# Kernel tuning notes

Hardware: AMD Instinct MI355X
Metric: run time of the kernel (lower is better)

## Reference

```python
import jax, jax.numpy as jnp
import numpy as np

NUM_V = 500_000      # num (k-1)-simplices (vertices)
NUM_E = 1_500_000    # num k-simplices (edges)
NNZ = 2 * NUM_E      # 2 oriented incidences per edge
D_FEAT = 64


def setup_inputs() -> dict:
    key = jax.random.key(0)
    k1, k2, k3, k4 = jax.random.split(key, 4)
    simplex_features = jax.random.normal(k1, (NUM_E, D_FEAT), dtype=jnp.float32)
    # oriented incidence values are +/-1
    boundary_values = jnp.sign(jax.random.normal(k2, (NNZ,), dtype=jnp.float32))
    boundary_values = jnp.where(boundary_values == 0, 1.0, boundary_values)
    boundary_rows = jax.random.randint(k3, (NNZ,), 0, NUM_V, dtype=jnp.int32)
    boundary_cols = jax.random.randint(k4, (NNZ,), 0, NUM_E, dtype=jnp.int32)
    return {
        "simplex_features": simplex_features,
        "boundary_values": boundary_values,
        "boundary_rows": boundary_rows,
        "boundary_cols": boundary_cols,
        "num_out": NUM_V,
    }


def reference(simplex_features, boundary_values, boundary_rows, boundary_cols, num_out):
    # SpMM: out[r, :] += val * features[c, :] over all nonzeros (r, c, val).
    gathered = boundary_values[:, None] * simplex_features[boundary_cols]  # [nnz, d]
    out = jax.ops.segment_sum(gathered, boundary_rows, num_segments=num_out)  # [num_out, d]
    return out
```

## Files before the change

### kernel.cpp

```cpp
#include <hip/hip_runtime.h>

#define D_FEAT 64
#define SCAN_BLOCK 256
#define SCAN_ITEMS 16
#define SCAN_CHUNK (SCAN_BLOCK * SCAN_ITEMS)
#define SCANB_THREADS 1024

#define EMPTY_SLOT 0xFFFFFFFFu
#define ROW_CAP 16

typedef unsigned int u32;
typedef float f4 __attribute__((ext_vector_type(4)));


__device__ __forceinline__ void slow_claim(u32* __restrict__ line, u32 entry, u32 h,
                                           u32 r, u32* __restrict__ spill,
                                           u32* __restrict__ spill_cnt, u32 spill_cap) {
    for (u32 p = 1; p < ROW_CAP; ++p) {
        u32 old = atomicCAS(line + ((h + p) & (ROW_CAP - 1)), EMPTY_SLOT, entry);
        if (old == EMPTY_SLOT) return;
    }
    u32 kk = atomicAdd(spill_cnt, 1u);
    if (kk < spill_cap) { spill[2 * kk] = r; spill[2 * kk + 1] = entry; }
}

__global__ __launch_bounds__(256) void scatter_cas_kernel(
    const int* __restrict__ rows, const int* __restrict__ cols,
    const float* __restrict__ vals, u32* __restrict__ slots,
    u32* __restrict__ spill, u32* __restrict__ spill_cnt, int nnz, u32 spill_cap) {
    long long i4 = (long long)blockIdx.x * blockDim.x + threadIdx.x;
    long long base = i4 * 4;
    if (base >= nnz) return;

    if (base + 3 < nnz) {
        int4 rr = *(const int4*)(rows + base);
        int4 cc = *(const int4*)(cols + base);
        float4 vv = *(const float4*)(vals + base);

        u32 e0 = (u32)cc.x | (vv.x < 0.f ? 0x80000000u : 0u);
        u32 e1 = (u32)cc.y | (vv.y < 0.f ? 0x80000000u : 0u);
        u32 e2 = (u32)cc.z | (vv.z < 0.f ? 0x80000000u : 0u);
        u32 e3 = (u32)cc.w | (vv.w < 0.f ? 0x80000000u : 0u);

        u32* L0 = slots + (size_t)rr.x * ROW_CAP;
        u32* L1 = slots + (size_t)rr.y * ROW_CAP;
        u32* L2 = slots + (size_t)rr.z * ROW_CAP;
        u32* L3 = slots + (size_t)rr.w * ROW_CAP;

        u32 h0 = (u32)(base + 0) & (ROW_CAP - 1);
        u32 h1 = (u32)(base + 1) & (ROW_CAP - 1);
        u32 h2 = (u32)(base + 2) & (ROW_CAP - 1);
        u32 h3 = (u32)(base + 3) & (ROW_CAP - 1);

        u32 o0 = atomicCAS(L0 + h0, EMPTY_SLOT, e0);
        u32 o1 = atomicCAS(L1 + h1, EMPTY_SLOT, e1);
        u32 o2 = atomicCAS(L2 + h2, EMPTY_SLOT, e2);
        u32 o3 = atomicCAS(L3 + h3, EMPTY_SLOT, e3);

        if (o0 != EMPTY_SLOT) slow_claim(L0, e0, h0, (u32)rr.x, spill, spill_cnt, spill_cap);
        if (o1 != EMPTY_SLOT) slow_claim(L1, e1, h1, (u32)rr.y, spill, spill_cnt, spill_cap);
        if (o2 != EMPTY_SLOT) slow_claim(L2, e2, h2, (u32)rr.z, spill, spill_cnt, spill_cap);
        if (o3 != EMPTY_SLOT) slow_claim(L3, e3, h3, (u32)rr.w, spill, spill_cnt, spill_cap);
    } else {
        for (int k = 0; k < 4; ++k) {
            long long e = base + k;
            if (e >= nnz) break;
            int r = rows[e];
            u32 entry = (u32)cols[e] | (vals[e] < 0.f ? 0x80000000u : 0u);
            u32* line = slots + (size_t)r * ROW_CAP;
            u32 h = (u32)e & (ROW_CAP - 1);
            u32 old = atomicCAS(line + h, EMPTY_SLOT, entry);
            if (old != EMPTY_SLOT) slow_claim(line, entry, h, (u32)r, spill, spill_cnt, spill_cap);
        }
    }
}

__global__ __launch_bounds__(256) void gather_cas_kernel(
    const f4* __restrict__ feat4, const u32* __restrict__ slots,
    f4* __restrict__ out4, int numV) {
    long long tid = (long long)blockIdx.x * blockDim.x + threadIdx.x;
    long long wid = tid >> 6;
    int lane = (int)(tid & 63);
    int g = lane >> 4;
    int s = lane & 15;
    long long row = wid * 4 + g;
    if (row >= numV) return;

    const u32* line = slots + row * (long long)ROW_CAP;
    uint4 q0 = *(const uint4*)(line + 0);
    uint4 q1 = *(const uint4*)(line + 4);
    uint4 q2 = *(const uint4*)(line + 8);
    uint4 q3 = *(const uint4*)(line + 12);

    const f4 z = {0.f, 0.f, 0.f, 0.f};
    f4 acc = z;

#define GATHER8(Ea, Eb, Ec, Ed, Ee, Ef, Eg2, Eh)                                   \
    {                                                                              \
        f4 fa = z, fb = z, fc = z, fd = z, fe = z, ff = z, fg = z, fh = z;         \
        if (Ea != EMPTY_SLOT) fa = feat4[(size_t)(Ea & 0x7fffffffu) * 16 + s];     \
        if (Eb != EMPTY_SLOT) fb = feat4[(size_t)(Eb & 0x7fffffffu) * 16 + s];     \
        if (Ec != EMPTY_SLOT) fc = feat4[(size_t)(Ec & 0x7fffffffu) * 16 + s];     \
        if (Ed != EMPTY_SLOT) fd = feat4[(size_t)(Ed & 0x7fffffffu) * 16 + s];     \
        if (Ee != EMPTY_SLOT) fe = feat4[(size_t)(Ee & 0x7fffffffu) * 16 + s];     \
        if (Ef != EMPTY_SLOT) ff = feat4[(size_t)(Ef & 0x7fffffffu) * 16 + s];     \
        if (Eg2 != EMPTY_SLOT) fg = feat4[(size_t)(Eg2 & 0x7fffffffu) * 16 + s];   \
        if (Eh != EMPTY_SLOT) fh = feat4[(size_t)(Eh & 0x7fffffffu) * 16 + s];     \
        acc += fa * ((Ea >> 31) ? -1.f : 1.f);                                     \
        acc += fb * ((Eb >> 31) ? -1.f : 1.f);                                     \
        acc += fc * ((Ec >> 31) ? -1.f : 1.f);                                     \
        acc += fd * ((Ed >> 31) ? -1.f : 1.f);                                     \
        acc += fe * ((Ee >> 31) ? -1.f : 1.f);                                     \
        acc += ff * ((Ef >> 31) ? -1.f : 1.f);                                     \
        acc += fg * ((Eg2 >> 31) ? -1.f : 1.f);                                    \
        acc += fh * ((Eh >> 31) ? -1.f : 1.f);                                     \
    }
    GATHER8(q0.x, q0.y, q0.z, q0.w, q1.x, q1.y, q1.z, q1.w)
    GATHER8(q2.x, q2.y, q2.z, q2.w, q3.x, q3.y, q3.z, q3.w)
#undef GATHER8

    __builtin_nontemporal_store(acc, &out4[row * 16 + s]);
}

__global__ __launch_bounds__(256) void spill_apply_kernel(
    const float* __restrict__ feat, const u32* __restrict__ spill,
    const u32* __restrict__ spill_cnt, float* __restrict__ out, u32 spill_cap) {
    u32 total = *spill_cnt;
    if (total > spill_cap) total = spill_cap;
    int lane = threadIdx.x & 63;
    u32 wid = (blockIdx.x * blockDim.x + threadIdx.x) >> 6;
    u32 nw = (gridDim.x * blockDim.x) >> 6;
    for (u32 i = wid; i < total; i += nw) {
        u32 r = spill[2 * i];
        u32 e = spill[2 * i + 1];
        float f = feat[(size_t)(e & 0x7fffffffu) * D_FEAT + lane];
        atomicAdd(&out[(size_t)r * D_FEAT + lane], (e & 0x80000000u) ? -f : f);
    }
}


__global__ __launch_bounds__(256) void count_kernel(const int* __restrict__ rows,
                                                    u32* __restrict__ cnt, int nnz) {
    int e = blockIdx.x * blockDim.x + threadIdx.x;
    if (e < nnz) atomicAdd(&cnt[rows[e]], 1u);
}

__global__ __launch_bounds__(SCAN_BLOCK) void scanA_kernel(const u32* __restrict__ cnt,
                                                           u32* __restrict__ bsums, int n) {
    int t = threadIdx.x, b = blockIdx.x;
    int i0 = b * SCAN_CHUNK + t * SCAN_ITEMS;
    u32 s = 0;
#pragma unroll
    for (int k = 0; k < SCAN_ITEMS; ++k) {
        int i = i0 + k;
        if (i < n) s += cnt[i];
    }
    __shared__ u32 red[SCAN_BLOCK];
    red[t] = s;
    __syncthreads();
    for (int d = SCAN_BLOCK / 2; d > 0; d >>= 1) {
        if (t < d) red[t] += red[t + d];
        __syncthreads();
    }
    if (t == 0) bsums[b] = red[0];
}

__global__ __launch_bounds__(SCANB_THREADS) void scanB_kernel(u32* __restrict__ bsums, int nb,
                                                              u32* __restrict__ off, int numV,
                                                              u32 nnz) {
    int t = threadIdx.x;
    __shared__ u32 tmp[SCANB_THREADS];
    u32 v = (t < nb) ? bsums[t] : 0u;
    tmp[t] = v;
    __syncthreads();
    for (int d = 1; d < SCANB_THREADS; d <<= 1) {
        u32 x = (t >= d) ? tmp[t - d] : 0u;
        __syncthreads();
        tmp[t] += x;
        __syncthreads();
    }
    if (t < nb) bsums[t] = tmp[t] - v;
    if (t == 0) off[numV] = nnz;
}

__global__ __launch_bounds__(SCAN_BLOCK) void scanC_kernel(const u32* __restrict__ cnt,
                                                           const u32* __restrict__ bsums,
                                                           u32* __restrict__ off,
                                                           u32* __restrict__ cursor, int n) {
    int t = threadIdx.x, b = blockIdx.x;
    int i0 = b * SCAN_CHUNK + t * SCAN_ITEMS;
    u32 s = 0;
#pragma unroll
    for (int k = 0; k < SCAN_ITEMS; ++k) {
        int i = i0 + k;
        if (i < n) s += cnt[i];
    }
    __shared__ u32 tmp[SCAN_BLOCK];
    tmp[t] = s;
    __syncthreads();
    for (int d = 1; d < SCAN_BLOCK; d <<= 1) {
        u32 x = (t >= d) ? tmp[t - d] : 0u;
        __syncthreads();
        tmp[t] += x;
        __syncthreads();
    }
    u32 run = bsums[b] + (tmp[t] - s);
    for (int k = 0; k < SCAN_ITEMS; ++k) {
        int i = i0 + k;
        if (i < n) {
            off[i] = run;
            cursor[i] = run;
            run += cnt[i];
        }
    }
}

__global__ __launch_bounds__(256) void scatter_kernel(const int* __restrict__ rows,
                                                      const int* __restrict__ cols,
                                                      const float* __restrict__ vals,
                                                      u32* __restrict__ cursor,
                                                      u32* __restrict__ packed, int nnz) {
    int e = blockIdx.x * blockDim.x + threadIdx.x;
    if (e >= nnz) return;
    int r = rows[e];
    u32 pos = atomicAdd(&cursor[r], 1u);
    u32 entry = (u32)cols[e] | (vals[e] < 0.f ? 0x80000000u : 0u);
    packed[pos] = entry;
}

__global__ __launch_bounds__(256) void gather_kernel(const float* __restrict__ feat,
                                                     const u32* __restrict__ off,
                                                     const u32* __restrict__ packed,
                                                     float* __restrict__ out, int numV) {
    long long tid = (long long)blockIdx.x * blockDim.x + threadIdx.x;
    long long wid = tid >> 6;
    int lane = (int)(tid & 63);
    if (wid >= numV) return;

    u32 s = off[wid];
    u32 e = off[wid + 1];
    float acc = 0.f;

    for (u32 base = s; base < e; base += 64) {
        int cnt = (int)min(64u, e - base);
        u32 ent = (lane < cnt) ? packed[base + lane] : 0u;
        for (int j0 = 0; j0 < cnt; j0 += 4) {
            float f[4], sg[4];
#pragma unroll
            for (int k = 0; k < 4; ++k) {
                int j = j0 + k;
                u32 ej = __shfl(ent, j);
                long long c = (long long)(ej & 0x7fffffffu);
                sg[k] = (ej >> 31) ? -1.f : 1.f;
                f[k] = (j < cnt) ? feat[c * D_FEAT + lane] : 0.f;
            }
#pragma unroll
            for (int k = 0; k < 4; ++k) acc = fmaf(sg[k], f[k], acc);
        }
    }
    out[wid * D_FEAT + lane] = acc;
}

__global__ __launch_bounds__(256) void atomic_fallback_kernel(
    const float* __restrict__ feat, const float* __restrict__ vals,
    const int* __restrict__ rows, const int* __restrict__ cols,
    float* __restrict__ out, long long nnz) {
    long long tid = (long long)blockIdx.x * blockDim.x + threadIdx.x;
    long long e = tid >> 6;
    int d = (int)(tid & 63);
    if (e >= nnz) return;
    float f = feat[(long long)cols[e] * D_FEAT + d];
    atomicAdd(out + (long long)rows[e] * D_FEAT + d, vals[e] * f);
}

extern "C" void kernel_launch(void* const* d_in, const int* in_sizes, int n_in,
                              void* d_out, int out_size, void* d_ws, size_t ws_size,
                              hipStream_t stream) {
    const float* feat = (const float*)d_in[0];
    const float* vals = (const float*)d_in[1];
    const int*   rows = (const int*)d_in[2];
    const int*   cols = (const int*)d_in[3];
    float*       out  = (float*)d_out;

    int nnz  = in_sizes[1];
    int numV = out_size / D_FEAT;

    {
        const u32 spcap = 1u << 20;
        size_t needT1 = (16 + (size_t)numV * ROW_CAP + 2 * (size_t)spcap) * sizeof(u32);
        if (ws_size >= needT1) {
            u32* ws        = (u32*)d_ws;
            u32* spill_cnt = ws;
            u32* slots     = ws + 16;
            u32* spill     = slots + (size_t)numV * ROW_CAP;

            hipMemsetAsync(spill_cnt, 0, 16 * sizeof(u32), stream);
            hipMemsetAsync(slots, 0xFF, (size_t)numV * ROW_CAP * sizeof(u32), stream);

            long long nth4 = ((long long)nnz + 3) / 4;
            int nb4 = (int)((nth4 + 255) / 256);
            scatter_cas_kernel<<<nb4, 256, 0, stream>>>(rows, cols, vals, slots,
                                                        spill, spill_cnt, nnz, spcap);

            long long waves = ((long long)numV + 3) / 4;
            long long gthreads = waves * 64;
            int gblocks = (int)((gthreads + 255) / 256);
            gather_cas_kernel<<<gblocks, 256, 0, stream>>>((const f4*)feat, slots,
                                                           (f4*)out, numV);
            spill_apply_kernel<<<64, 256, 0, stream>>>(feat, spill, spill_cnt, out, spcap);
            return;
        }
    }

    int nScanBlocks = (numV + SCAN_CHUNK - 1) / SCAN_CHUNK;
    size_t need = ((size_t)(numV + 1) + numV + numV + SCANB_THREADS + nnz) * sizeof(u32);

    if (ws_size < need || nScanBlocks > SCANB_THREADS) {
        hipMemsetAsync(d_out, 0, (size_t)out_size * sizeof(float), stream);
        long long total = (long long)nnz * D_FEAT;
        long long nblk = (total + 255) / 256;
        atomic_fallback_kernel<<<(dim3)((unsigned)nblk), 256, 0, stream>>>(
            feat, vals, rows, cols, out, nnz);
        return;
    }

    u32* ws     = (u32*)d_ws;
    u32* off    = ws;
    u32* cursor = off + (numV + 1);
    u32* cnt    = cursor + numV;
    u32* bsums  = cnt + numV;
    u32* packed = bsums + SCANB_THREADS;

    hipMemsetAsync(cnt, 0, (size_t)numV * sizeof(u32), stream);

    int nb256 = (nnz + 255) / 256;
    count_kernel<<<nb256, 256, 0, stream>>>(rows, cnt, nnz);
    scanA_kernel<<<nScanBlocks, SCAN_BLOCK, 0, stream>>>(cnt, bsums, numV);
    scanB_kernel<<<1, SCANB_THREADS, 0, stream>>>(bsums, nScanBlocks, off, numV, (u32)nnz);
    scanC_kernel<<<nScanBlocks, SCAN_BLOCK, 0, stream>>>(cnt, bsums, off, cursor, numV);
    scatter_kernel<<<nb256, 256, 0, stream>>>(rows, cols, vals, cursor, packed, nnz);

    long long gthreads = (long long)numV * 64;
    long long gblocks  = (gthreads + 255) / 256;
    gather_kernel<<<(dim3)((unsigned)gblocks), 256, 0, stream>>>(feat, off, packed, out, numV);
}
```

Measured before the change: 752.4 us.

## Replace global CAS hash scatter with two-pass radix binning into row slot tables

Adds a radix binning pass that groups nonzeros by high bits of the row into per-bucket arrays using shared-memory histograms and one global atomic per bucket per block. A second kernel builds the per-row slot tables in shared memory for half-buckets and writes them out with coalesced vector stores, replacing the per-entry global atomicCAS scatter and the large 0xFF memset of the slot array. This trades the random global atomics for an extra pass over an intermediate 8-byte-per-entry binned buffer. Overflow entries still go to the spill path.

```diff
diff --git a/kernel.cpp b/kernel.cpp
--- a/kernel.cpp
+++ b/kernel.cpp
@@ -9,8 +9,131 @@
 #define EMPTY_SLOT 0xFFFFFFFFu
 #define ROW_CAP 16
 
+#define RADIX_SHIFT 10
+#define ROWS_PER_BUCKET 1024
+#define HALF_ROWS 512
+#define RADIX_NB_MAX 512
+#define EPB 4096
+#define CURSOR_STRIDE 16
+
 typedef unsigned int u32;
+typedef unsigned long long u64;
 typedef float f4 __attribute__((ext_vector_type(4)));
+
+
+__global__ __launch_bounds__(256) void radix_bin_kernel(
+    const int* __restrict__ rows, const int* __restrict__ cols,
+    const float* __restrict__ vals, u32* __restrict__ cursor,
+    u64* __restrict__ binned, u32* __restrict__ spill, u32* __restrict__ spill_cnt,
+    int nnz, int NB, u32 CAP, u32 spill_cap) {
+    __shared__ u32 hist[RADIX_NB_MAX];
+    __shared__ u32 sbase[RADIX_NB_MAX];
+    int t = threadIdx.x;
+    long long b0 = (long long)blockIdx.x * EPB;
+
+    for (int i = t; i < RADIX_NB_MAX; i += 256) hist[i] = 0;
+    __syncthreads();
+
+    u32 pack[16];
+    u64 ent[16];
+#pragma unroll
+    for (int k = 0; k < 4; ++k) {
+        long long i = b0 + (long long)t * 4 + (long long)k * 1024;
+        int4 rr = {0, 0, 0, 0}, cc = {0, 0, 0, 0};
+        float4 vv = {0.f, 0.f, 0.f, 0.f};
+        bool v4 = (i + 3 < nnz);
+        if (v4) {
+            rr = *(const int4*)(rows + i);
+            cc = *(const int4*)(cols + i);
+            vv = *(const float4*)(vals + i);
+        }
+#define DO_EDGE(J, RJ, CJ, VJ)                                                      \
+        {                                                                           \
+            long long e = i + J;                                                    \
+            int r = RJ, c = CJ; float v = VJ;                                       \
+            bool valid = v4;                                                        \
+            if (!v4) {                                                              \
+                valid = (e < nnz);                                                  \
+                if (valid) { r = rows[e]; c = cols[e]; v = vals[e]; }               \
+                else { r = 0; c = 0; v = 0.f; }                                     \
+            }                                                                       \
+            u32 digit = (u32)r >> RADIX_SHIFT;                                      \
+            u32 rank = 0;                                                           \
+            if (valid) rank = atomicAdd(&hist[digit], 1u);                          \
+            pack[k * 4 + J] = digit | (rank << 9) | (valid ? 0x80000000u : 0u);     \
+            ent[k * 4 + J] = ((u64)((u32)r & (ROWS_PER_BUCKET - 1)) << 32) |        \
+                             (u64)((u32)c | (v < 0.f ? 0x80000000u : 0u));          \
+        }
+        DO_EDGE(0, rr.x, cc.x, vv.x)
+        DO_EDGE(1, rr.y, cc.y, vv.y)
+        DO_EDGE(2, rr.z, cc.z, vv.z)
+        DO_EDGE(3, rr.w, cc.w, vv.w)
+#undef DO_EDGE
+    }
+    __syncthreads();
+
+    for (int i = t; i < RADIX_NB_MAX; i += 256) {
+        u32 c = hist[i];
+        sbase[i] = c ? atomicAdd(&cursor[i * CURSOR_STRIDE], c) : 0u;
+    }
+    __syncthreads();
+
+#pragma unroll
+    for (int q = 0; q < 16; ++q) {
+        u32 p = pack[q];
+        if (p & 0x80000000u) {
+            u32 digit = p & 0x1FFu;
+            u32 pos = sbase[digit] + ((p >> 9) & 0xFFFu);
+            if (pos < CAP) {
+                binned[(size_t)digit * CAP + pos] = ent[q];
+            } else {
+                u32 kk = atomicAdd(spill_cnt, 1u);
+                u32 r = (digit << RADIX_SHIFT) | (u32)(ent[q] >> 32);
+                if (kk < spill_cap) { spill[2 * kk] = r; spill[2 * kk + 1] = (u32)ent[q]; }
+            }
+        }
+    }
+}
+
+__global__ __launch_bounds__(256) void radix_place_kernel(
+    const u64* __restrict__ binned, const u32* __restrict__ cursor,
+    u32* __restrict__ slots, u32* __restrict__ spill, u32* __restrict__ spill_cnt,
+    u32 CAP, u32 spill_cap) {
+    __shared__ u32 table[HALF_ROWS * ROW_CAP];
+    __shared__ u32 rcnt[HALF_ROWS];
+    int t = threadIdx.x;
+    int b = blockIdx.x >> 1;
+    int h = blockIdx.x & 1;
+
+    for (int i = t; i < HALF_ROWS * ROW_CAP; i += 256) table[i] = EMPTY_SLOT;
+    for (int i = t; i < HALF_ROWS; i += 256) rcnt[i] = 0;
+    __syncthreads();
+
+    u32 count = cursor[b * CURSOR_STRIDE];
+    if (count > CAP) count = CAP;
+    const u64* src = binned + (size_t)b * CAP;
+    for (u32 i = t; i < count; i += 256) {
+        u64 e = src[i];
+        u32 rowlo = (u32)(e >> 32);
+        if ((int)(rowlo >> 9) == h) {
+            u32 rl = rowlo & (HALF_ROWS - 1);
+            u32 k = atomicAdd(&rcnt[rl], 1u);
+            if (k < ROW_CAP) {
+                table[rl * ROW_CAP + k] = (u32)e;
+            } else {
+                u32 kk = atomicAdd(spill_cnt, 1u);
+                u32 r = ((u32)b << RADIX_SHIFT) | rowlo;
+                if (kk < spill_cap) { spill[2 * kk] = r; spill[2 * kk + 1] = (u32)e; }
+            }
+        }
+    }
+    __syncthreads();
+
+    u32 rowbase = ((u32)b << RADIX_SHIFT) | ((u32)h << 9);
+    uint4* dst = (uint4*)(slots + (size_t)rowbase * ROW_CAP);
+    const uint4* srcT = (const uint4*)table;
+    for (int i = t; i < HALF_ROWS * ROW_CAP / 4; i += 256) dst[i] = srcT[i];
+}
 
 
 __device__ __forceinline__ void slow_claim(u32* __restrict__ line, u32 entry, u32 h,
@@ -286,6 +409,46 @@
     int numV = out_size / D_FEAT;
 
     {
+        int NB = (numV + ROWS_PER_BUCKET - 1) >> RADIX_SHIFT;
+        const u32 spcap = 1u << 20;
+        if (NB >= 1 && NB <= RADIX_NB_MAX && nnz >= 0) {
+            u32 CAP = ((u32)(nnz / NB) * 2u + 1024u + 63u) & ~63u;
+            size_t rowsPad = (size_t)NB << RADIX_SHIFT;
+            size_t metaU   = 16 + (size_t)RADIX_NB_MAX * CURSOR_STRIDE;
+            size_t slotsU  = rowsPad * ROW_CAP;
+            size_t binnedU = (size_t)NB * CAP * 2;
+            size_t need = (metaU + slotsU + binnedU + 2 * (size_t)spcap) * sizeof(u32);
+            if (ws_size >= need) {
+                u32* ws        = (u32*)d_ws;
+                u32* spill_cnt = ws;
+                u32* cursor    = ws + 16;
+                u32* slots     = ws + metaU;
+                u64* binned    = (u64*)(slots + slotsU);
+                u32* spill     = (u32*)(binned + (size_t)NB * CAP);
+
+                hipMemsetAsync(ws, 0, metaU * sizeof(u32), stream);
+
+                if (nnz > 0) {
+                    int nb1 = (int)(((long long)nnz + EPB - 1) / EPB);
+                    radix_bin_kernel<<<nb1, 256, 0, stream>>>(
+                        rows, cols, vals, cursor, binned, spill, spill_cnt,
+                        nnz, NB, CAP, spcap);
+                }
+                radix_place_kernel<<<NB * 2, 256, 0, stream>>>(
+                    binned, cursor, slots, spill, spill_cnt, CAP, spcap);
+
+                long long waves = ((long long)numV + 3) / 4;
+                long long gthreads = waves * 64;
+                int gblocks = (int)((gthreads + 255) / 256);
+                gather_cas_kernel<<<gblocks, 256, 0, stream>>>((const f4*)feat, slots,
+                                                               (f4*)out, numV);
+                spill_apply_kernel<<<64, 256, 0, stream>>>(feat, spill, spill_cnt, out, spcap);
+                return;
+            }
+        }
+    }
+
+    {
         const u32 spcap = 1u << 20;
         size_t needT1 = (16 + (size_t)numV * ROW_CAP + 2 * (size_t)spcap) * sizeof(u32);
         if (ws_size >= needT1) {
```

New measurement: 662.8 us. 11.9% less time.
